# Kernel optimization log

Hardware: AMD Instinct MI355X
Metric: run time of the kernel (lower is better)

Reference implementation:

```python
import jax, jax.numpy as jnp
import numpy as np

S, B_BOX, N_CLASS = 7, 2, 20
L_COORD, L_NOOBJ = 5.0, 0.5
BATCH = 4096
C = 5 * B_BOX + N_CLASS  # 30


def setup_inputs() -> dict:
    key = jax.random.key(0)
    k1, k2, k3, k4 = jax.random.split(key, 4)
    # coords/w/h/classes strictly positive (sqrt is applied to raw values)
    y = jax.random.uniform(k1, (BATCH, S, S, C), minval=0.05, maxval=0.95, dtype=jnp.float32)
    # confidence channels must be exactly 0/1 (mask tests == 1)
    conf0 = jax.random.bernoulli(k3, 0.3, (BATCH, S, S)).astype(jnp.float32)
    conf1 = jax.random.bernoulli(k4, 0.3, (BATCH, S, S)).astype(jnp.float32)
    y = y.at[..., 0].set(conf0).at[..., 5].set(conf1)
    y_h = jax.random.uniform(k2, (BATCH, S, S, C), minval=0.05, maxval=0.95, dtype=jnp.float32)
    return {"y": y, "y_h": y_h}


def _loss(y, y_h):
    b_sz = y.shape[0]
    conf_idx = np.arange(B_BOX) * 5  # [0, 5]
    y_conf = y[..., conf_idx]        # [B,S,S,b]
    yh_conf = y_h[..., conf_idx]
    mf = (y_conf == 1.0).astype(y.dtype)  # obj mask per box, constant wrt grads
    dconf = (y_conf - yh_conf) ** 2
    loss_obj = jnp.sum(dconf * mf)
    loss_noobj = jnp.sum(dconf * (1.0 - mf))

    loss_coord = jnp.zeros((), y.dtype)
    loss_prob = jnp.zeros((), y.dtype)
    for k in range(B_BOX):  # static small loop over boxes
        mk = mf[..., k]  # [B,S,S]
        base = 5 * k
        dxy = (y[..., base + 1] - y_h[..., base + 1]) ** 2 \
            + (y[..., base + 2] - y_h[..., base + 2]) ** 2
        dwh = (jnp.sqrt(y[..., base + 3]) - jnp.sqrt(y_h[..., base + 3])) ** 2 \
            + (jnp.sqrt(y[..., base + 4]) - jnp.sqrt(y_h[..., base + 4])) ** 2
        loss_coord = loss_coord + jnp.sum((dxy + dwh) * mk)

        # prob term: slice from k*5+5 to end (faithful to original, for k=0 this
        # includes box-2's 5 entries), softmax over the masked batch dimension.
        tail = y[..., base + 5:]
        tail_h = y_h[..., base + 5:]
        mkb = mk[..., None]  # [B,S,S,1]
        neg = jnp.where(mkb > 0, tail_h, -jnp.inf)
        m = jnp.max(neg, axis=0)                       # [S,S,Ct]
        m_safe = jnp.where(jnp.isfinite(m), m, 0.0)    # guard empty columns
        p = jnp.exp(tail_h - m_safe) * mkb
        denom = jnp.sum(p, axis=0)
        sm = p / jnp.where(denom > 0, denom, 1.0)
        loss_prob = loss_prob + jnp.sum((tail - sm) ** 2 * mkb)

    loss = loss_obj + L_NOOBJ * loss_noobj + L_COORD * loss_coord + loss_prob
    return loss / b_sz


def reference(y, y_h):
    return _loss(y, y_h)
```

## Files before the change

### kernel.cpp

```cpp
#include <hip/hip_runtime.h>
#include <math.h>

#define CC 30
#define NBATCH 4096
#define NIJ 49
#define NPAIR 1225
#define PSTR 7352
#define F4TOT (PSTR / 4)
#define THREADS 512
#define SLABF4 1470
#define SLABF  5880


__global__ __launch_bounds__(THREADS)
void yolo_main(const float* __restrict__ y, const float* __restrict__ yh,
               float* __restrict__ scal, float* __restrict__ parts, int nwg)
{
    __shared__ __align__(16) float tY[2][SLABF];
    __shared__ __align__(16) float tH[2][SLABF];
    __shared__ float scr[4][8];

    const int tid = threadIdx.x;
    const int wg  = blockIdx.x;
    const int bpw = NBATCH / nwg;
    const int nslab = bpw >> 2;

    const int i0 = tid, i1 = tid + 512;
    const int i2r = tid + 1024;
    const int i2  = (i2r < SLABF4) ? i2r : (SLABF4 - 1);
    const bool w2 = (i2r < SLABF4);

    int  ijv[3], cv[3], pr[3];
    bool val[3];
    #pragma unroll
    for (int i = 0; i < 3; i++) {
        int p = tid + i * THREADS;
        val[i] = (p < NPAIR);
        pr[i]  = p;
        int pp = val[i] ? p : 0;
        ijv[i] = pp / 25;
        cv[i]  = 5 + pp % 25;
    }

    float D0[3] = {0,0,0}, B0[3] = {0,0,0}, C0[3] = {0,0,0};
    float D1[3] = {0,0,0}, B1[3] = {0,0,0}, C1[3] = {0,0,0};
    float obj = 0.f, noobj = 0.f, coord = 0.f, tt = 0.f;

    const float4* Yg = (const float4*)y;
    const float4* Hg = (const float4*)yh;

    {
        const size_t f4 = (size_t)((wg * bpw) >> 2) * SLABF4;
        float4 a0 = Yg[f4+i0], a1 = Yg[f4+i1], a2 = Yg[f4+i2];
        float4 b0 = Hg[f4+i0], b1 = Hg[f4+i1], b2 = Hg[f4+i2];
        float4* dY = (float4*)tY[0];
        float4* dH = (float4*)tH[0];
        dY[i0] = a0; dY[i1] = a1; if (w2) dY[i2] = a2;
        dH[i0] = b0; dH[i1] = b1; if (w2) dH[i2] = b2;
    }
    __syncthreads();

    for (int s = 0; s < nslab; s++) {
        const float* cy = tY[s & 1];
        const float* ch = tH[s & 1];
        const bool pf = (s + 1 < nslab);
        float4 ry0, ry1, ry2, rh0, rh1, rh2;
        if (pf) {
            const size_t nf4 = (size_t)((wg * bpw + (s+1)*4) >> 2) * SLABF4;
            ry0 = Yg[nf4+i0]; ry1 = Yg[nf4+i1]; ry2 = Yg[nf4+i2];
            rh0 = Hg[nf4+i0]; rh1 = Hg[nf4+i1]; rh2 = Hg[nf4+i2];
        }

        if (tid < 4 * NIJ) {
            const int base = tid * CC;
            float y0 = cy[base],     h0 = ch[base];
            float y5 = cy[base + 5], h5 = ch[base + 5];
            float d0 = y0 - h0; d0 *= d0;
            float d5 = y5 - h5; d5 *= d5;
            const bool m0 = (y0 == 1.0f), m1 = (y5 == 1.0f);
            obj   += (m0 ? d0 : 0.f) + (m1 ? d5 : 0.f);
            noobj += (m0 ? 0.f : d0) + (m1 ? 0.f : d5);
            if (m0) {
                float a  = cy[base + 1] - ch[base + 1];
                float b2 = cy[base + 2] - ch[base + 2];
                float c1 = sqrtf(cy[base + 3]) - sqrtf(ch[base + 3]);
                float c2 = sqrtf(cy[base + 4]) - sqrtf(ch[base + 4]);
                coord += a * a + b2 * b2 + c1 * c1 + c2 * c2;
            }
            if (m1) {
                float a  = cy[base + 6] - ch[base + 6];
                float b2 = cy[base + 7] - ch[base + 7];
                float c1 = sqrtf(cy[base + 8]) - sqrtf(ch[base + 8]);
                float c2 = sqrtf(cy[base + 9]) - sqrtf(ch[base + 9]);
                coord += a * a + b2 * b2 + c1 * c1 + c2 * c2;
            }
        }

        #pragma unroll
        for (int b = 0; b < 4; b++) {
            #pragma unroll
            for (int i = 0; i < 3; i++) {
                if (!val[i]) continue;
                const int cb = b * 1470 + ijv[i] * CC;
                const float w0 = (cy[cb] == 1.0f) ? 1.f : 0.f;
                const float wk = (cv[i] >= 10 && cy[cb + 5] == 1.0f) ? 1.f : 0.f;
                const float t  = cy[cb + cv[i]];
                const float th = ch[cb + cv[i]];
                const float e  = __expf(th);
                const float te = t * e, ee = e * e, t2 = t * t;
                D0[i] = fmaf(e,  w0, D0[i]);
                B0[i] = fmaf(te, w0, B0[i]);
                C0[i] = fmaf(ee, w0, C0[i]);
                D1[i] = fmaf(e,  wk, D1[i]);
                B1[i] = fmaf(te, wk, B1[i]);
                C1[i] = fmaf(ee, wk, C1[i]);
                tt = fmaf(t2, w0 + wk, tt);
            }
        }

        if (pf) {
            float4* dY = (float4*)tY[(s + 1) & 1];
            float4* dH = (float4*)tH[(s + 1) & 1];
            dY[i0] = ry0; dY[i1] = ry1; if (w2) dY[i2] = ry2;
            dH[i0] = rh0; dH[i1] = rh1; if (w2) dH[i2] = rh2;
        }
        __syncthreads();
    }

    float* pp = parts + (size_t)wg * PSTR;
    #pragma unroll
    for (int i = 0; i < 3; i++) {
        if (!val[i]) continue;
        const int p = pr[i];
        pp[p]            = D0[i];
        pp[NPAIR + p]    = B0[i];
        pp[2*NPAIR + p]  = C0[i];
        pp[3*NPAIR + p]  = D1[i];
        pp[4*NPAIR + p]  = B1[i];
        pp[5*NPAIR + p]  = C1[i];
    }

    const int lane = tid & 63, wv = tid >> 6;
    #pragma unroll
    for (int off = 32; off > 0; off >>= 1) {
        obj   += __shfl_down(obj,   off);
        noobj += __shfl_down(noobj, off);
        coord += __shfl_down(coord, off);
        tt    += __shfl_down(tt,    off);
    }
    if (lane == 0) { scr[0][wv] = obj; scr[1][wv] = noobj; scr[2][wv] = coord; scr[3][wv] = tt; }
    __syncthreads();
    if (tid < 4) {
        float sacc = 0.f;
        #pragma unroll
        for (int w = 0; w < THREADS / 64; w++) sacc += scr[tid][w];
        scal[wg * 4 + tid] = sacc;
    }
}

__global__ __launch_bounds__(512)
void yolo_reduce(const float* __restrict__ parts, float* __restrict__ parts2, int nwg)
{
    const int lane = threadIdx.x & 63;
    const int sub  = threadIdx.x >> 6;
    const int f4i  = blockIdx.x * 64 + lane;
    const int cy   = blockIdx.y;
    const int wpc  = nwg >> 3;
    const int wps  = wpc >> 3;

    float4 s = make_float4(0.f, 0.f, 0.f, 0.f);
    if (f4i < F4TOT) {
        const float* q = parts + (size_t)(cy * wpc + sub * wps) * PSTR + f4i * 4;
        for (int w = 0; w < wps; ++w) {
            float4 a = *(const float4*)q;
            s.x += a.x; s.y += a.y; s.z += a.z; s.w += a.w;
            q += PSTR;
        }
    }
    __shared__ float4 sred[8][64];
    sred[sub][lane] = s;
    __syncthreads();
    if (threadIdx.x < 64 && f4i < F4TOT) {
        float4 t = sred[0][lane];
        #pragma unroll
        for (int c = 1; c < 8; c++) {
            float4 a = sred[c][lane];
            t.x += a.x; t.y += a.y; t.z += a.z; t.w += a.w;
        }
        *(float4*)(parts2 + (size_t)cy * PSTR + f4i * 4) = t;
    }
}

__global__ __launch_bounds__(1024)
void yolo_final(const float* __restrict__ parts2, const float* __restrict__ scal,
                float* __restrict__ out, int nwg)
{
    float v = 0.f;

    for (int s = threadIdx.x; s < NPAIR; s += 1024) {
        const int cidx = s % 25;
        float D0 = 0, B0 = 0, C0 = 0, D1 = 0, B1 = 0, C1 = 0;
        #pragma unroll
        for (int c = 0; c < 8; c++) {
            const float* t = parts2 + (size_t)c * PSTR;
            D0 += t[s];           B0 += t[NPAIR + s];   C0 += t[2*NPAIR + s];
            D1 += t[3*NPAIR + s]; B1 += t[4*NPAIR + s]; C1 += t[5*NPAIR + s];
        }
        if (D0 > 0.f) v += C0 / (D0 * D0) - 2.f * B0 / D0;
        if (cidx >= 5 && D1 > 0.f) v += C1 / (D1 * D1) - 2.f * B1 / D1;
    }

    const float4* s4 = (const float4*)scal;
    for (int w = threadIdx.x; w < nwg; w += 1024) {
        float4 a = s4[w];
        v += a.x + 0.5f * a.y + 5.0f * a.z + a.w;
    }

    __shared__ float sred[16];
    #pragma unroll
    for (int off = 32; off > 0; off >>= 1) v += __shfl_down(v, off);
    const int lane = threadIdx.x & 63, wv = threadIdx.x >> 6;
    if (lane == 0) sred[wv] = v;
    __syncthreads();
    if (threadIdx.x == 0) {
        float tot = 0.f;
        #pragma unroll
        for (int w = 0; w < 16; w++) tot += sred[w];
        out[0] = tot / (float)NBATCH;
    }
}

extern "C" void kernel_launch(void* const* d_in, const int* in_sizes, int n_in,
                              void* d_out, int out_size, void* d_ws, size_t ws_size,
                              hipStream_t stream)
{
    const float* y  = (const float*)d_in[0];
    const float* yh = (const float*)d_in[1];
    float* out    = (float*)d_out;
    float* scal   = (float*)d_ws;
    float* parts2 = (float*)((char*)d_ws + 8192);
    float* parts  = (float*)((char*)d_ws + 243456);

    const size_t per_wg = (size_t)PSTR * sizeof(float);
    int nwg;
    if      (ws_size >= 243456 + 256 * per_wg) nwg = 256;
    else if (ws_size >= 243456 + 128 * per_wg) nwg = 128;
    else                                       nwg = 64;

    yolo_main<<<nwg, THREADS, 0, stream>>>(y, yh, scal, parts, nwg);
    dim3 g2((F4TOT + 63) / 64, 8);
    yolo_reduce<<<g2, 512, 0, stream>>>(parts, parts2, nwg);
    yolo_final<<<1, 1024, 0, stream>>>(parts2, scal, out, nwg);
}
```

Measured before the change: 27.48 us.

## Fold per-column softmax finalisation into reduce kernel, shrink final kernel

The reduce kernel now splits work by column groups (25 blocks of 49 columns) instead of by float4 chunks and batch slices. Each block sums all workgroup partials for its columns and evaluates the softmax loss term directly, writing one scalar per block. The single-block final kernel then only sums 25 scalars plus the per-workgroup scalars, instead of reading 8x7352 partials and doing divisions serially. The trade-off is less parallelism in the reduce stage (25 blocks, scalar strided loads instead of float4) in exchange for removing the serial tail work.

```diff
diff --git a/kernel.cpp b/kernel.cpp
--- a/kernel.cpp
+++ b/kernel.cpp
@@ -6,7 +6,6 @@
 #define NIJ 49
 #define NPAIR 1225
 #define PSTR 7352
-#define F4TOT (PSTR / 4)
 #define THREADS 512
 #define SLABF4 1470
 #define SLABF  5880
@@ -159,75 +158,70 @@
 }
 
 __global__ __launch_bounds__(512)
-void yolo_reduce(const float* __restrict__ parts, float* __restrict__ parts2, int nwg)
-{
-    const int lane = threadIdx.x & 63;
-    const int sub  = threadIdx.x >> 6;
-    const int f4i  = blockIdx.x * 64 + lane;
-    const int cy   = blockIdx.y;
-    const int wpc  = nwg >> 3;
-    const int wps  = wpc >> 3;
-
-    float4 s = make_float4(0.f, 0.f, 0.f, 0.f);
-    if (f4i < F4TOT) {
-        const float* q = parts + (size_t)(cy * wpc + sub * wps) * PSTR + f4i * 4;
+void yolo_reduce(const float* __restrict__ parts, float* __restrict__ cont, int nwg)
+{
+    const int tid  = threadIdx.x;
+    const int lane = tid & 63;
+    const int sub  = tid >> 6;
+    const int s0   = blockIdx.x * 49;
+    const int wps  = nwg >> 3;
+
+    float D0=0,B0=0,C0=0,D1=0,B1=0,C1=0;
+    if (lane < 49) {
+        const float* q = parts + (size_t)(sub * wps) * PSTR + s0 + lane;
         for (int w = 0; w < wps; ++w) {
-            float4 a = *(const float4*)q;
-            s.x += a.x; s.y += a.y; s.z += a.z; s.w += a.w;
+            D0 += q[0];
+            B0 += q[NPAIR];
+            C0 += q[2*NPAIR];
+            D1 += q[3*NPAIR];
+            B1 += q[4*NPAIR];
+            C1 += q[5*NPAIR];
             q += PSTR;
         }
     }
-    __shared__ float4 sred[8][64];
-    sred[sub][lane] = s;
-    __syncthreads();
-    if (threadIdx.x < 64 && f4i < F4TOT) {
-        float4 t = sred[0][lane];
-        #pragma unroll
-        for (int c = 1; c < 8; c++) {
-            float4 a = sred[c][lane];
-            t.x += a.x; t.y += a.y; t.z += a.z; t.w += a.w;
-        }
-        *(float4*)(parts2 + (size_t)cy * PSTR + f4i * 4) = t;
-    }
-}
-
-__global__ __launch_bounds__(1024)
-void yolo_final(const float* __restrict__ parts2, const float* __restrict__ scal,
+    __shared__ float sred[8][6][50];
+    if (lane < 49) {
+        sred[sub][0][lane] = D0; sred[sub][1][lane] = B0; sred[sub][2][lane] = C0;
+        sred[sub][3][lane] = D1; sred[sub][4][lane] = B1; sred[sub][5][lane] = C1;
+    }
+    __syncthreads();
+
+    float v = 0.f;
+    if (tid < 49) {
+        float d0=0,b0=0,c0=0,d1=0,b1=0,c1=0;
+        #pragma unroll
+        for (int k = 0; k < 8; k++) {
+            d0 += sred[k][0][tid]; b0 += sred[k][1][tid]; c0 += sred[k][2][tid];
+            d1 += sred[k][3][tid]; b1 += sred[k][4][tid]; c1 += sred[k][5][tid];
+        }
+        const int cidx = (s0 + tid) % 25;
+        if (d0 > 0.f) v += c0 / (d0 * d0) - 2.f * b0 / d0;
+        if (cidx >= 5 && d1 > 0.f) v += c1 / (d1 * d1) - 2.f * b1 / d1;
+    }
+    if (tid < 64) {
+        #pragma unroll
+        for (int off = 32; off > 0; off >>= 1) v += __shfl_down(v, off);
+        if (tid == 0) cont[blockIdx.x] = v;
+    }
+}
+
+__global__ __launch_bounds__(256)
+void yolo_final(const float* __restrict__ cont, const float* __restrict__ scal,
                 float* __restrict__ out, int nwg)
 {
-    float v = 0.f;
-
-    for (int s = threadIdx.x; s < NPAIR; s += 1024) {
-        const int cidx = s % 25;
-        float D0 = 0, B0 = 0, C0 = 0, D1 = 0, B1 = 0, C1 = 0;
-        #pragma unroll
-        for (int c = 0; c < 8; c++) {
-            const float* t = parts2 + (size_t)c * PSTR;
-            D0 += t[s];           B0 += t[NPAIR + s];   C0 += t[2*NPAIR + s];
-            D1 += t[3*NPAIR + s]; B1 += t[4*NPAIR + s]; C1 += t[5*NPAIR + s];
-        }
-        if (D0 > 0.f) v += C0 / (D0 * D0) - 2.f * B0 / D0;
-        if (cidx >= 5 && D1 > 0.f) v += C1 / (D1 * D1) - 2.f * B1 / D1;
-    }
-
+    const int tid = threadIdx.x;
+    float v = (tid < 25) ? cont[tid] : 0.f;
     const float4* s4 = (const float4*)scal;
-    for (int w = threadIdx.x; w < nwg; w += 1024) {
+    for (int w = tid; w < nwg; w += 256) {
         float4 a = s4[w];
         v += a.x + 0.5f * a.y + 5.0f * a.z + a.w;
     }
-
-    __shared__ float sred[16];
+    __shared__ float sr[4];
     #pragma unroll
     for (int off = 32; off > 0; off >>= 1) v += __shfl_down(v, off);
-    const int lane = threadIdx.x & 63, wv = threadIdx.x >> 6;
-    if (lane == 0) sred[wv] = v;
-    __syncthreads();
-    if (threadIdx.x == 0) {
-        float tot = 0.f;
-        #pragma unroll
-        for (int w = 0; w < 16; w++) tot += sred[w];
-        out[0] = tot / (float)NBATCH;
-    }
+    if ((tid & 63) == 0) sr[tid >> 6] = v;
+    __syncthreads();
+    if (tid == 0) out[0] = (sr[0] + sr[1] + sr[2] + sr[3]) / (float)NBATCH;
 }
 
 extern "C" void kernel_launch(void* const* d_in, const int* in_sizes, int n_in,
@@ -236,19 +230,18 @@
 {
     const float* y  = (const float*)d_in[0];
     const float* yh = (const float*)d_in[1];
-    float* out    = (float*)d_out;
-    float* scal   = (float*)d_ws;
-    float* parts2 = (float*)((char*)d_ws + 8192);
-    float* parts  = (float*)((char*)d_ws + 243456);
+    float* out   = (float*)d_out;
+    float* scal  = (float*)d_ws;
+    float* cont  = (float*)((char*)d_ws + 4096);
+    float* parts = (float*)((char*)d_ws + 8192);
 
     const size_t per_wg = (size_t)PSTR * sizeof(float);
     int nwg;
-    if      (ws_size >= 243456 + 256 * per_wg) nwg = 256;
-    else if (ws_size >= 243456 + 128 * per_wg) nwg = 128;
-    else                                       nwg = 64;
+    if      (ws_size >= 8192 + 256 * per_wg) nwg = 256;
+    else if (ws_size >= 8192 + 128 * per_wg) nwg = 128;
+    else                                     nwg = 64;
 
     yolo_main<<<nwg, THREADS, 0, stream>>>(y, yh, scal, parts, nwg);
-    dim3 g2((F4TOT + 63) / 64, 8);
-    yolo_reduce<<<g2, 512, 0, stream>>>(parts, parts2, nwg);
-    yolo_final<<<1, 1024, 0, stream>>>(parts2, scal, out, nwg);
-}
+    yolo_reduce<<<25, 512, 0, stream>>>(parts, cont, nwg);
+    yolo_final<<<1, 256, 0, stream>>>(cont, scal, out, nwg);
+}
```

Measured after the change: 35.02 us. +27.5%, slower.
